# Kernel tuning notes

Measured on AMD Instinct MI355X. Metric: run time of the kernel, lower is better.

The kernel has to match this reference:

```python
import jax, jax.numpy as jnp
import numpy as np

BATCH, T, IN_DIM = 256, 1024, 96
N_UNITS, N_CLASSES = 256, 10
EPS, BETA, GAMMA = 0.01, 0.5, 0.0


def setup_inputs() -> dict:
    key = jax.random.key(0)
    k = jax.random.split(key, 7)
    # Xavier-ish scales for linear layers; unit gaussian for C, B (gaussian_init_ std=1)
    return {
        "x":   jax.random.normal(k[0], (BATCH, T, IN_DIM), dtype=jnp.float32),
        "E_w": jax.random.normal(k[1], (N_UNITS, IN_DIM), dtype=jnp.float32) * (2.0 / (IN_DIM + N_UNITS)) ** 0.5,
        "E_b": jnp.zeros((N_UNITS,), dtype=jnp.float32),
        "C":   jax.random.normal(k[2], (N_UNITS, N_UNITS), dtype=jnp.float32) / N_UNITS ** 0.5,
        "B":   jax.random.normal(k[3], (N_UNITS, N_UNITS), dtype=jnp.float32) / N_UNITS ** 0.5,
        "D_w": jax.random.normal(k[4], (N_CLASSES, N_UNITS), dtype=jnp.float32) * (2.0 / (N_UNITS + N_CLASSES)) ** 0.5,
        "D_b": jnp.zeros((N_CLASSES,), dtype=jnp.float32),
    }


def reference(x, E_w, E_b, C, B, D_w, D_b):
    # Invariant recurrence matrices (the torch code rebuilds these every step)
    I = jnp.eye(N_UNITS, dtype=x.dtype)
    A  = BETA * (C - C.T) + (1.0 - BETA) * (C + C.T) - GAMMA * I
    Dm = BETA * (B - B.T) + (1.0 - BETA) * (B + B.T) - GAMMA * I

    # Input projection for all timesteps at once: [B, T, N]
    z = jnp.einsum("btf,nf->btn", x, E_w) + E_b

    def step(h, z_t):  # h: [B, N], z_t: [B, N]
        h = h + EPS * (h @ Dm) + EPS * jnp.tanh(h @ A + z_t)
        return h, None

    h0 = jnp.zeros((x.shape[0], N_UNITS), dtype=x.dtype)
    h, _ = jax.lax.scan(step, h0, jnp.swapaxes(z, 0, 1))  # scan over T

    return h @ D_w.T + D_b  # [B, n_classes]
```

## Files before the change

kernel.cpp:

```cpp
#include <hip/hip_runtime.h>

#define BATCH 256
#define TT 1024
#define IN_DIM 96
#define NU 256
#define NC 10
#define EPS 0.01f
#define BETA 0.5f
#define GAMMA 0.0f

typedef _Float16 f16x8 __attribute__((ext_vector_type(8)));
typedef _Float16 f16x4 __attribute__((ext_vector_type(4)));
typedef float f32x4 __attribute__((ext_vector_type(4)));

#define ZP_BYTES ((size_t)TT * 16 * 256 * 16 * 2)
#define WSW_OFF  ZP_BYTES
#define WSW_BYTES ((size_t)16384 * 16)
#define ESW_OFF  (WSW_OFF + WSW_BYTES)

__global__ void prep_w(const float* __restrict__ C, const float* __restrict__ B,
                       _Float16* __restrict__ Wsw) {
    int u = blockIdx.x * 256 + threadIdx.x;
    int l = u & 63;
    int i = (u >> 6) & 1;
    int c = (u >> 7) & 7;
    int mat = (u >> 10) & 1;
    int w = u >> 11;
    int n = w * 32 + i * 16 + (l & 15);
    int kb = c * 32 + (l >> 4) * 8;
    const float* M = mat ? C : B;
    float scale = mat ? 16.0f : EPS;
    f16x8 v;
#pragma unroll
    for (int j = 0; j < 8; j++) {
        int k = kb + j;
        float m1 = M[k * NU + n];
        float m2 = M[n * NU + k];
        float val = BETA * (m1 - m2) + (1.0f - BETA) * (m1 + m2)
                    - ((k == n) ? GAMMA : 0.0f);
        v[j] = (_Float16)(val * scale);
    }
    ((f16x8*)Wsw)[u] = v;
}

__global__ void prep_e(const float* __restrict__ Ew, _Float16* __restrict__ Esw) {
    int u = blockIdx.x * 256 + threadIdx.x;
    int l = u & 63;
    int i = (u >> 6) & 3;
    int wc = u >> 8;
    int c = wc % 3;
    int w = wc / 3;
    int n = w * 64 + i * 16 + (l & 15);
    int kb = c * 32 + (l >> 4) * 8;
    f16x8 v;
#pragma unroll
    for (int j = 0; j < 8; j++)
        v[j] = (_Float16)Ew[n * IN_DIM + kb + j];
    ((f16x8*)Esw)[u] = v;
}

__global__ __launch_bounds__(256) void zproj(const float* __restrict__ x,
                                             const float* __restrict__ Eb,
                                             const _Float16* __restrict__ Esw,
                                             _Float16* __restrict__ zp) {
    __shared__ __align__(16) _Float16 zt[2][256 * 24];
    int tid = threadIdx.x;
    int l = tid & 63, wz = tid >> 6, m = l & 15, q = l >> 4;
    int bb = blockIdx.x & 15, tb = blockIdx.x >> 4;
    int t0 = tb * 16, B0 = bb * 16;

    f16x8 ef[3][4];
    const f16x8* Ep = (const f16x8*)Esw;
#pragma unroll
    for (int c = 0; c < 3; c++)
#pragma unroll
        for (int i = 0; i < 4; i++)
            ef[c][i] = Ep[((wz * 3 + c) * 4 + i) * 64 + l];
    float eb[4];
#pragma unroll
    for (int i = 0; i < 4; i++) eb[i] = Eb[wz * 64 + i * 16 + m];

    const float* xbase = x + (size_t)(B0 + m) * TT * IN_DIM + q * 8;

    for (int t = 0; t < 16; t++) {
        f16x8 af[3];
#pragma unroll
        for (int c = 0; c < 3; c++) {
            const float* px = xbase + (size_t)(t0 + t) * IN_DIM + c * 32;
            float4 v0 = *(const float4*)px;
            float4 v1 = *(const float4*)(px + 4);
            f16x8 a;
            a[0] = (_Float16)v0.x; a[1] = (_Float16)v0.y;
            a[2] = (_Float16)v0.z; a[3] = (_Float16)v0.w;
            a[4] = (_Float16)v1.x; a[5] = (_Float16)v1.y;
            a[6] = (_Float16)v1.z; a[7] = (_Float16)v1.w;
            af[c] = a;
        }
        f32x4 acc[4];
#pragma unroll
        for (int i = 0; i < 4; i++) { f32x4 e4 = {eb[i], eb[i], eb[i], eb[i]}; acc[i] = e4; }
#pragma unroll
        for (int c = 0; c < 3; c++)
#pragma unroll
            for (int i = 0; i < 4; i++)
                acc[i] = __builtin_amdgcn_mfma_f32_16x16x32_f16(af[c], ef[c][i], acc[i], 0, 0, 0);

        _Float16* zb = zt[t & 1];
#pragma unroll
        for (int i = 0; i < 4; i++) {
            f16x4 o = {(_Float16)acc[i][0], (_Float16)acc[i][1],
                       (_Float16)acc[i][2], (_Float16)acc[i][3]};
            *(f16x4*)&zb[(wz * 64 + i * 16 + m) * 24 + q * 4] = o;
        }
        __syncthreads();
        {
            _Float16* src = &zb[tid * 24];
            f16x8 s0 = *(f16x8*)src;
            f16x8 s1 = *(f16x8*)(src + 8);
            _Float16* dst = zp + ((((size_t)(t0 + t) * 16) + bb) * 256 + tid) * 16;
            *(f16x8*)dst = s0;
            *(f16x8*)(dst + 8) = s1;
        }
        __syncthreads();
    }
}


__device__ __forceinline__ void load_z2(f16x4 zc[2][2],
                                        const _Float16* __restrict__ zp,
                                        int tb, int wg, size_t voff0, size_t voff1) {
#pragma unroll
    for (int s = 0; s < 2; s++) {
        int ts = tb + s; ts = (ts > TT - 1) ? TT - 1 : ts;
        const _Float16* pz = zp + ((size_t)ts * 16 + wg) * 4096;
        zc[s][0] = *(const f16x4*)(pz + voff0);
        zc[s][1] = *(const f16x4*)(pz + voff1);
    }
}

__device__ __forceinline__ void step_fn(const _Float16* __restrict__ hb,
                                        _Float16* __restrict__ hn,
                                        const f16x8 wd[8][2], const f16x8 wa[8][2],
                                        float hm[8], const f16x4 zs[2],
                                        int m, int q, int w) {
    f32x4 faccD[2], faccA[2];
    f32x4 zero4 = {0.f, 0.f, 0.f, 0.f};
#pragma unroll
    for (int i = 0; i < 2; i++) {
        faccD[i] = zero4;
        f32x4 zi = {(float)zs[i][0], (float)zs[i][1],
                    (float)zs[i][2], (float)zs[i][3]};
        faccA[i] = zi;
    }

#pragma unroll
    for (int c = 0; c < 8; c++) {
        f16x8 af = *(const f16x8*)&hb[m * 264 + c * 32 + q * 8];
#pragma unroll
        for (int i = 0; i < 2; i++) {
            faccD[i] = __builtin_amdgcn_mfma_f32_16x16x32_f16(af, wd[c][i], faccD[i], 0, 0, 0);
            faccA[i] = __builtin_amdgcn_mfma_f32_16x16x32_f16(af, wa[c][i], faccA[i], 0, 0, 0);
        }
    }

#pragma unroll
    for (int i = 0; i < 2; i++) {
        int n = w * 32 + i * 16 + m;
#pragma unroll
        for (int r = 0; r < 4; r++) {
            int row = q * 4 + r;
            float xin = faccA[i][r];
            float e = __builtin_amdgcn_exp2f(xin * 2.8853900817779268f);
            float R = __builtin_amdgcn_rcpf(e + 1.0f);
            float s = hm[i * 4 + r] + faccD[i][r];
            hm[i * 4 + r] = s + (EPS * 0.0625f) - (2.0f * EPS * 0.0625f) * R;
            hn[row * 264 + n] = (_Float16)hm[i * 4 + r];
        }
    }
    __syncthreads();
}

__global__ __launch_bounds__(512, 2) void recur(const _Float16* __restrict__ Wsw,
                                                const _Float16* __restrict__ zp,
                                                const float* __restrict__ Dw,
                                                const float* __restrict__ Db,
                                                float* __restrict__ out) {
    __shared__ __align__(16) _Float16 hbuf0[16 * 264];
    __shared__ __align__(16) _Float16 hbuf1[16 * 264];
    __shared__ float Yep[16 * 257];
    int tid = threadIdx.x;
    int l = tid & 63, w = tid >> 6, m = l & 15, q = l >> 4;
    int wg = blockIdx.x;

    f16x8 wd[8][2], wa[8][2];
    const f16x8* Wp = (const f16x8*)Wsw;
#pragma unroll
    for (int c = 0; c < 8; c++)
#pragma unroll
        for (int i = 0; i < 2; i++) {
            wd[c][i] = Wp[(((w * 2 + 0) * 8 + c) * 2 + i) * 64 + l];
            wa[c][i] = Wp[(((w * 2 + 1) * 8 + c) * 2 + i) * 64 + l];
        }
#pragma unroll
    for (int c = 0; c < 8; c++)
#pragma unroll
        for (int i = 0; i < 2; i++)
            asm volatile("" : "+v"(wd[c][i]), "+v"(wa[c][i]));

    float hm[8];
#pragma unroll
    for (int e = 0; e < 8; e++) hm[e] = 0.0f;
    for (int idx = tid; idx < 16 * 264; idx += 512) hbuf0[idx] = (_Float16)0.0f;

    size_t voff0 = (size_t)(w * 32 + m) * 16 + q * 4;
    size_t voff1 = voff0 + 256;
    f16x4 zA[2][2], zB[2][2];
    load_z2(zA, zp, 0, wg, voff0, voff1);
    load_z2(zB, zp, 2, wg, voff0, voff1);
    __syncthreads();

    for (int t = 0; t < TT; t += 4) {
        step_fn(hbuf0, hbuf1, wd, wa, hm, zA[0], m, q, w);
        step_fn(hbuf1, hbuf0, wd, wa, hm, zA[1], m, q, w);
        load_z2(zA, zp, t + 4, wg, voff0, voff1);
        step_fn(hbuf0, hbuf1, wd, wa, hm, zB[0], m, q, w);
        step_fn(hbuf1, hbuf0, wd, wa, hm, zB[1], m, q, w);
        load_z2(zB, zp, t + 6, wg, voff0, voff1);
    }

#pragma unroll
    for (int i = 0; i < 2; i++)
#pragma unroll
        for (int r = 0; r < 4; r++)
            Yep[(q * 4 + r) * 257 + w * 32 + i * 16 + m] = 16.0f * hm[i * 4 + r];
    __syncthreads();
    if (tid < 160) {
        int rr = tid / 10, c = tid - rr * 10;
        float s = Db[c];
        for (int k = 0; k < 256; k++) s += Yep[rr * 257 + k] * Dw[c * 256 + k];
        out[(wg * 16 + rr) * 10 + c] = s;
    }
}

extern "C" void kernel_launch(void* const* d_in, const int* in_sizes, int n_in,
                              void* d_out, int out_size, void* d_ws, size_t ws_size,
                              hipStream_t stream) {
    const float* x  = (const float*)d_in[0];
    const float* Ew = (const float*)d_in[1];
    const float* Eb = (const float*)d_in[2];
    const float* C  = (const float*)d_in[3];
    const float* B  = (const float*)d_in[4];
    const float* Dw = (const float*)d_in[5];
    const float* Db = (const float*)d_in[6];
    float* out = (float*)d_out;

    char* ws = (char*)d_ws;
    _Float16* zp  = (_Float16*)(ws);
    _Float16* Wsw = (_Float16*)(ws + WSW_OFF);
    _Float16* Esw = (_Float16*)(ws + ESW_OFF);

    hipLaunchKernelGGL(prep_w, dim3(64), dim3(256), 0, stream, C, B, Wsw);
    hipLaunchKernelGGL(prep_e, dim3(12), dim3(256), 0, stream, Ew, Esw);
    hipLaunchKernelGGL(zproj, dim3(1024), dim3(256), 0, stream, x, Eb, Esw, zp);
    hipLaunchKernelGGL(recur, dim3(16), dim3(512), 0, stream, Wsw, zp, Dw, Db, out);
}
```

Baseline: 1.075 ms.

## Transpose MFMA operands so each lane stores contiguous h and z vectors

Swaps the A/B operands of the MFMA calls so the accumulator holds a transposed tile. Each lane now writes four consecutive hidden units as one f16x4 store to LDS instead of four scattered scalar stores, and the z-projection buffer layout is changed to match. The 2*log2(e) tanh scaling is folded into the A, E and bias weights, and the +EPS/16 constant moves into the D accumulator init, which removes per-element multiplies from the serial recurrence. One redundant __syncthreads in zproj is also removed. The main risks are that the double-buffered zt now depends on its alternation for correctness, and that pre-scaling the weights changes fp16 rounding slightly.

```diff
diff --git a/kernel.cpp b/kernel.cpp
--- a/kernel.cpp
+++ b/kernel.cpp
@@ -8,12 +8,13 @@
 #define EPS 0.01f
 #define BETA 0.5f
 #define GAMMA 0.0f
+#define TWOLOG2E 2.8853900817779268f
 
 typedef _Float16 f16x8 __attribute__((ext_vector_type(8)));
 typedef _Float16 f16x4 __attribute__((ext_vector_type(4)));
 typedef float f32x4 __attribute__((ext_vector_type(4)));
 
-#define ZP_BYTES ((size_t)TT * 16 * 256 * 16 * 2)
+#define ZP_BYTES ((size_t)TT * 16 * 16 * 256 * 2)
 #define WSW_OFF  ZP_BYTES
 #define WSW_BYTES ((size_t)16384 * 16)
 #define ESW_OFF  (WSW_OFF + WSW_BYTES)
@@ -29,7 +30,7 @@
     int n = w * 32 + i * 16 + (l & 15);
     int kb = c * 32 + (l >> 4) * 8;
     const float* M = mat ? C : B;
-    float scale = mat ? 16.0f : EPS;
+    float scale = mat ? (16.0f * TWOLOG2E) : EPS;
     f16x8 v;
 #pragma unroll
     for (int j = 0; j < 8; j++) {
@@ -55,7 +56,7 @@
     f16x8 v;
 #pragma unroll
     for (int j = 0; j < 8; j++)
-        v[j] = (_Float16)Ew[n * IN_DIM + kb + j];
+        v[j] = (_Float16)(Ew[n * IN_DIM + kb + j] * TWOLOG2E);
     ((f16x8*)Esw)[u] = v;
 }
 
@@ -63,7 +64,7 @@
                                              const float* __restrict__ Eb,
                                              const _Float16* __restrict__ Esw,
                                              _Float16* __restrict__ zp) {
-    __shared__ __align__(16) _Float16 zt[2][256 * 24];
+    __shared__ __align__(16) _Float16 zt[2][16 * 264];
     int tid = threadIdx.x;
     int l = tid & 63, wz = tid >> 6, m = l & 15, q = l >> 4;
     int bb = blockIdx.x & 15, tb = blockIdx.x >> 4;
@@ -76,9 +77,14 @@
 #pragma unroll
         for (int i = 0; i < 4; i++)
             ef[c][i] = Ep[((wz * 3 + c) * 4 + i) * 64 + l];
-    float eb[4];
-#pragma unroll
-    for (int i = 0; i < 4; i++) eb[i] = Eb[wz * 64 + i * 16 + m];
+    f32x4 ebv[4];
+#pragma unroll
+    for (int i = 0; i < 4; i++) {
+        float4 b4 = *(const float4*)&Eb[wz * 64 + i * 16 + q * 4];
+        f32x4 e4 = {b4.x * TWOLOG2E, b4.y * TWOLOG2E,
+                    b4.z * TWOLOG2E, b4.w * TWOLOG2E};
+        ebv[i] = e4;
+    }
 
     const float* xbase = x + (size_t)(B0 + m) * TT * IN_DIM + q * 8;
 
@@ -98,30 +104,29 @@
         }
         f32x4 acc[4];
 #pragma unroll
-        for (int i = 0; i < 4; i++) { f32x4 e4 = {eb[i], eb[i], eb[i], eb[i]}; acc[i] = e4; }
+        for (int i = 0; i < 4; i++) acc[i] = ebv[i];
 #pragma unroll
         for (int c = 0; c < 3; c++)
 #pragma unroll
             for (int i = 0; i < 4; i++)
-                acc[i] = __builtin_amdgcn_mfma_f32_16x16x32_f16(af[c], ef[c][i], acc[i], 0, 0, 0);
+                acc[i] = __builtin_amdgcn_mfma_f32_16x16x32_f16(ef[c][i], af[c], acc[i], 0, 0, 0);
 
         _Float16* zb = zt[t & 1];
 #pragma unroll
         for (int i = 0; i < 4; i++) {
             f16x4 o = {(_Float16)acc[i][0], (_Float16)acc[i][1],
                        (_Float16)acc[i][2], (_Float16)acc[i][3]};
-            *(f16x4*)&zb[(wz * 64 + i * 16 + m) * 24 + q * 4] = o;
+            *(f16x4*)&zb[m * 264 + wz * 64 + i * 16 + q * 4] = o;
         }
         __syncthreads();
         {
-            _Float16* src = &zb[tid * 24];
-            f16x8 s0 = *(f16x8*)src;
-            f16x8 s1 = *(f16x8*)(src + 8);
-            _Float16* dst = zp + ((((size_t)(t0 + t) * 16) + bb) * 256 + tid) * 16;
+            const _Float16* src = &zb[(tid >> 4) * 264 + (tid & 15) * 16];
+            f16x8 s0 = *(const f16x8*)src;
+            f16x8 s1 = *(const f16x8*)(src + 8);
+            _Float16* dst = zp + (((size_t)(t0 + t) * 16 + bb) * 4096) + tid * 16;
             *(f16x8*)dst = s0;
             *(f16x8*)(dst + 8) = s1;
         }
-        __syncthreads();
     }
 }
 
@@ -144,10 +149,10 @@
                                         float hm[8], const f16x4 zs[2],
                                         int m, int q, int w) {
     f32x4 faccD[2], faccA[2];
-    f32x4 zero4 = {0.f, 0.f, 0.f, 0.f};
+    f32x4 dinit = {EPS * 0.0625f, EPS * 0.0625f, EPS * 0.0625f, EPS * 0.0625f};
 #pragma unroll
     for (int i = 0; i < 2; i++) {
-        faccD[i] = zero4;
+        faccD[i] = dinit;
         f32x4 zi = {(float)zs[i][0], (float)zs[i][1],
                     (float)zs[i][2], (float)zs[i][3]};
         faccA[i] = zi;
@@ -158,24 +163,23 @@
         f16x8 af = *(const f16x8*)&hb[m * 264 + c * 32 + q * 8];
 #pragma unroll
         for (int i = 0; i < 2; i++) {
-            faccD[i] = __builtin_amdgcn_mfma_f32_16x16x32_f16(af, wd[c][i], faccD[i], 0, 0, 0);
-            faccA[i] = __builtin_amdgcn_mfma_f32_16x16x32_f16(af, wa[c][i], faccA[i], 0, 0, 0);
+            faccD[i] = __builtin_amdgcn_mfma_f32_16x16x32_f16(wd[c][i], af, faccD[i], 0, 0, 0);
+            faccA[i] = __builtin_amdgcn_mfma_f32_16x16x32_f16(wa[c][i], af, faccA[i], 0, 0, 0);
         }
     }
 
 #pragma unroll
     for (int i = 0; i < 2; i++) {
-        int n = w * 32 + i * 16 + m;
+        f16x4 o;
 #pragma unroll
         for (int r = 0; r < 4; r++) {
-            int row = q * 4 + r;
-            float xin = faccA[i][r];
-            float e = __builtin_amdgcn_exp2f(xin * 2.8853900817779268f);
+            float e = __builtin_amdgcn_exp2f(faccA[i][r]);
             float R = __builtin_amdgcn_rcpf(e + 1.0f);
             float s = hm[i * 4 + r] + faccD[i][r];
-            hm[i * 4 + r] = s + (EPS * 0.0625f) - (2.0f * EPS * 0.0625f) * R;
-            hn[row * 264 + n] = (_Float16)hm[i * 4 + r];
-        }
+            hm[i * 4 + r] = s - (2.0f * EPS * 0.0625f) * R;
+            o[r] = (_Float16)hm[i * 4 + r];
+        }
+        *(f16x4*)&hn[m * 264 + w * 32 + i * 16 + q * 4] = o;
     }
     __syncthreads();
 }
@@ -212,8 +216,8 @@
     for (int e = 0; e < 8; e++) hm[e] = 0.0f;
     for (int idx = tid; idx < 16 * 264; idx += 512) hbuf0[idx] = (_Float16)0.0f;
 
-    size_t voff0 = (size_t)(w * 32 + m) * 16 + q * 4;
-    size_t voff1 = voff0 + 256;
+    size_t voff0 = (size_t)m * 256 + w * 32 + q * 4;
+    size_t voff1 = voff0 + 16;
     f16x4 zA[2][2], zB[2][2];
     load_z2(zA, zp, 0, wg, voff0, voff1);
     load_z2(zB, zp, 2, wg, voff0, voff1);
@@ -232,7 +236,7 @@
     for (int i = 0; i < 2; i++)
 #pragma unroll
         for (int r = 0; r < 4; r++)
-            Yep[(q * 4 + r) * 257 + w * 32 + i * 16 + m] = 16.0f * hm[i * 4 + r];
+            Yep[m * 257 + w * 32 + i * 16 + q * 4 + r] = 16.0f * hm[i * 4 + r];
     __syncthreads();
     if (tid < 160) {
         int rr = tid / 10, c = tid - rr * 10;
```

New measurement: 1.131 ms. 1.05x slower.
